# Kernel optimization log

Hardware: AMD Instinct MI355X
Metric: run time of the kernel (lower is better)

The kernel has to match this reference:

```python
import jax, jax.numpy as jnp
import numpy as np

B, K1, N, DIMS = 512, 11, 5, 784  # K1 = K+1 samples per class incl. query
H = 512  # model_size


def _lstm(x_seq, W, U, b):
    """Keras-style LSTM, return_sequences=True.
    x_seq: [B, T, I]; W: [I, 4H]; U: [H, 4H]; b: [4H]. Gate order i,f,g,o.
    """
    units = U.shape[0]
    bsz = x_seq.shape[0]
    # precompute input projections for all timesteps: [T, B, 4H]
    xw = jnp.einsum('bti,ih->tbh', x_seq, W) + b

    def step(carry, xw_t):
        h, c = carry
        z = xw_t + h @ U  # [B, 4H]
        i, f, g, o = jnp.split(z, 4, axis=-1)
        i = jax.nn.sigmoid(i)
        f = jax.nn.sigmoid(f)
        g = jnp.tanh(g)
        o = jax.nn.sigmoid(o)
        c = f * c + i * g
        h = o * jnp.tanh(c)
        return (h, c), h

    init = (jnp.zeros((bsz, units), x_seq.dtype), jnp.zeros((bsz, units), x_seq.dtype))
    _, hs = jax.lax.scan(step, init, xw)  # hs: [T, B, H]
    return jnp.transpose(hs, (1, 0, 2))  # [B, T, H]


def setup_inputs() -> dict:
    key = jax.random.key(0)
    ks = jax.random.split(key, 8)
    return {
        'input_images': jax.random.normal(ks[0], (B, K1, N, DIMS), jnp.float32),
        'input_labels': jax.random.uniform(ks[1], (B, K1, N, N), jnp.float32),
        'W1': jax.random.normal(ks[2], (N + DIMS, 4 * H), jnp.float32) * 0.02,
        'U1': jax.random.normal(ks[3], (H, 4 * H), jnp.float32) * 0.02,
        'b1': jnp.zeros((4 * H,), jnp.float32),
        'W2': jax.random.normal(ks[4], (H, 4 * N), jnp.float32) * 0.02,
        'U2': jax.random.normal(ks[5], (N, 4 * N), jnp.float32) * 0.02,
        'b2': jnp.zeros((4 * N,), jnp.float32),
    }


def reference(input_images, input_labels, W1, U1, b1, W2, U2, b2):
    K = K1 - 1
    support_imgs = input_images[:, :K]               # [B, K, N, D]
    query_imgs = input_images[:, -1].reshape(-1, 1, N, DIMS)  # [B, 1, N, D]
    support_lbls = input_labels[:, :K]               # [B, K, N, N]
    concat_support = jnp.concatenate([support_imgs, support_lbls], axis=-1)
    zero_lbls = jnp.zeros((B, 1, N, N), input_images.dtype)
    concat_query = jnp.concatenate([query_imgs, zero_lbls], axis=-1)
    seq = jnp.concatenate([concat_support, concat_query], axis=1)  # [B, K1, N, N+D]
    seq = seq.reshape(-1, N * K1, N + DIMS)          # [B, T, N+D], T = N*K1
    x = _lstm(seq, W1, U1, b1)                       # [B, T, H]
    out = _lstm(x, W2, U2, b2)                       # [B, T, N]
    return out.reshape(-1, K1, N, N)
```

## Files before the change

kernel.cpp:

```cpp
#include <hip/hip_runtime.h>

typedef __attribute__((ext_vector_type(8))) __bf16 bf16x8;
typedef __attribute__((ext_vector_type(8))) unsigned short ushort8;
typedef __attribute__((ext_vector_type(4))) float f32x4;
typedef __attribute__((ext_vector_type(2))) unsigned long long u64x2;

#define DEVINL __device__ __forceinline__
#define RLX __ATOMIC_RELAXED
#define AGT __HIP_MEMORY_SCOPE_AGENT

constexpr int B_C    = 512;
constexpr int DIMS_C = 784;
constexpr int T_C    = 55;
constexpr int I0_C   = 789;
constexpr int KP_C   = 800;
constexpr int H_C    = 512;
constexpr int G4_C   = 2048;
constexpr int M1_C   = 28160;

constexpr size_t OFF_A    = 0;
constexpr size_t SZ_A     = (size_t)M1_C * KP_C * 2;
constexpr size_t OFF_W1T  = OFF_A + SZ_A;
constexpr size_t SZ_W1T   = (size_t)G4_C * KP_C * 2;
constexpr size_t OFF_U1T  = OFF_W1T + SZ_W1T;
constexpr size_t SZ_U1T   = (size_t)G4_C * H_C * 2;
constexpr size_t OFF_XW1  = OFF_U1T + SZ_U1T;
constexpr size_t SZ_XW1   = (size_t)M1_C * G4_C * 2;
constexpr size_t OFF_H    = OFF_XW1 + SZ_XW1;
constexpr size_t SZ_H     = (size_t)2 * B_C * H_C * 2;
constexpr size_t OFF_XMID = OFF_H + SZ_H;
constexpr size_t SZ_XMID  = (size_t)M1_C * H_C * 4;
constexpr size_t OFF_XW2  = OFF_XMID + SZ_XMID;
constexpr size_t SZ_XW2   = (size_t)M1_C * 20 * 4;
constexpr size_t OFF_W2T  = OFF_XW2 + SZ_XW2;
constexpr size_t SZ_W2T   = (size_t)20 * H_C * 4;
constexpr size_t OFF_CNT  = OFF_W2T + SZ_W2T;

DEVINL unsigned short f2bf(float f) {
  unsigned u = __builtin_bit_cast(unsigned, f);
  u += 0x7fffu + ((u >> 16) & 1u);
  return (unsigned short)(u >> 16);
}
DEVINL float sigm(float x) {
  return __builtin_amdgcn_rcpf(1.f + __builtin_amdgcn_exp2f(-1.4426950408889634f * x));
}
DEVINL float tanh_(float x) {
  return 2.f * __builtin_amdgcn_rcpf(1.f + __builtin_amdgcn_exp2f(-2.8853900817779268f * x)) - 1.f;
}
DEVINL void gl_lds16(const void* g, void* l) {
  __builtin_amdgcn_global_load_lds((const __attribute__((address_space(1))) void*)g,
                                   (__attribute__((address_space(3))) void*)l, 16, 0, 0);
}
DEVINL void gl_lds16_coh(const void* g, void* l) {
  __builtin_amdgcn_global_load_lds((const __attribute__((address_space(1))) void*)g,
                                   (__attribute__((address_space(3))) void*)l, 16, 0, 17);
}


__global__ void pack_a(const float* __restrict__ img, const float* __restrict__ lbl,
                       unsigned short* __restrict__ A) {
  int gid = blockIdx.x * blockDim.x + threadIdx.x;
  constexpr int CPR = KP_C / 8;
  if (gid >= M1_C * CPR) return;
  int r  = gid / CPR;
  int cc = gid - r * CPR;
  int t = r >> 9, b = r & 511;
  int k1 = t / 5, n = t - k1 * 5;
  int c0 = cc * 8;
  ushort8 v;
  if (c0 + 8 <= DIMS_C) {
    const float* p = img + ((size_t)((b * 11 + k1) * 5 + n)) * DIMS_C + c0;
    f32x4 x0 = *(const f32x4*)(p);
    f32x4 x1 = *(const f32x4*)(p + 4);
#pragma unroll
    for (int j = 0; j < 4; ++j) { v[j] = f2bf(x0[j]); v[4 + j] = f2bf(x1[j]); }
  } else {
#pragma unroll
    for (int j = 0; j < 8; ++j) {
      int c = c0 + j;
      float x = 0.f;
      if (c < DIMS_C) x = img[((size_t)((b * 11 + k1) * 5 + n)) * DIMS_C + c];
      else if (c < I0_C && k1 < 10) x = lbl[((size_t)((b * 11 + k1) * 5 + n)) * 5 + (c - DIMS_C)];
      v[j] = f2bf(x);
    }
  }
  *(ushort8*)(A + (size_t)r * KP_C + c0) = v;
}

__global__ void pack_w1t(const float* __restrict__ W1, unsigned short* __restrict__ W1T) {
  int gid = blockIdx.x * blockDim.x + threadIdx.x;
  if (gid >= G4_C * KP_C) return;
  int col = gid / KP_C, k = gid - col * KP_C;
  float x = (k < I0_C) ? W1[(size_t)k * G4_C + col] : 0.f;
  W1T[(size_t)col * KP_C + k] = f2bf(x);
}

__global__ void pack_u1t(const float* __restrict__ U1, unsigned short* __restrict__ U1T) {
  int gid = blockIdx.x * blockDim.x + threadIdx.x;
  if (gid >= G4_C * H_C) return;
  int col = gid / H_C, k = gid - col * H_C;
  U1T[(size_t)col * H_C + k] = f2bf(U1[(size_t)k * G4_C + col]);
}

__global__ void pack_w2t(const float* __restrict__ W2, float* __restrict__ W2T) {
  int gid = blockIdx.x * blockDim.x + threadIdx.x;
  if (gid >= 20 * H_C) return;
  int col = gid / H_C, k = gid - col * H_C;
  W2T[(size_t)col * H_C + k] = W2[(size_t)k * 20 + col];
}

__launch_bounds__(256, 2)
__global__ void gemm1(const unsigned short* __restrict__ A,
                      const unsigned short* __restrict__ Bt,
                      const float* __restrict__ bias,
                      _Float16* __restrict__ C)
{
  __shared__ unsigned short sA[2][128 * 32];
  __shared__ unsigned short sB[2][128 * 32];
  const int tid = threadIdx.x;
  const int w = tid >> 6, l = tid & 63;
  const int lo = l & 15, hi = l >> 4;
  const int wm = w >> 1, wn = w & 1;
  const int id = blockIdx.x;
  const int swz = (id & 7) * 440 + (id >> 3);
  const int by = swz >> 4;
  const int bx = swz & 15;

  const unsigned short* aSrc[2];
  const unsigned short* bSrc[2];
#pragma unroll
  for (int q = 0; q < 2; ++q) {
    int row = w * 32 + q * 16 + (l >> 2);
    int ch = l & 3;
    int sw = (row >> 1) & 3;
    aSrc[q] = A  + (size_t)(by * 128 + row) * KP_C + (ch ^ sw) * 8;
    bSrc[q] = Bt + (size_t)(bx * 128 + row) * KP_C + (ch ^ sw) * 8;
  }
  int aOff[4], bOff[4];
#pragma unroll
  for (int i = 0; i < 4; ++i) {
    int rA = wm * 64 + i * 16 + lo;
    aOff[i] = rA * 32 + ((hi ^ ((rA >> 1) & 3)) * 8);
    int rB = wn * 64 + i * 16 + lo;
    bOff[i] = rB * 32 + ((hi ^ ((rB >> 1) & 3)) * 8);
  }

  f32x4 acc[4][4];
#pragma unroll
  for (int i = 0; i < 4; ++i)
#pragma unroll
    for (int j = 0; j < 4; ++j) acc[i][j] = (f32x4){0.f, 0.f, 0.f, 0.f};

#define G1_STAGE(buf, ks)                                                  \
  {                                                                        \
    _Pragma("unroll")                                                      \
    for (int q = 0; q < 2; ++q) {                                          \
      gl_lds16(aSrc[q] + (ks) * 32, &sA[buf][w * 1024 + q * 512]);         \
      gl_lds16(bSrc[q] + (ks) * 32, &sB[buf][w * 1024 + q * 512]);         \
    }                                                                      \
  }

  G1_STAGE(0, 0);
  asm volatile("s_waitcnt vmcnt(0)" ::: "memory");
  __syncthreads();

  int cur = 0;
#pragma unroll 1
  for (int ks = 0; ks < KP_C / 32; ++ks) {
    if (ks < KP_C / 32 - 1) G1_STAGE(cur ^ 1, ks + 1);
    bf16x8 af[4], bfr[4];
#pragma unroll
    for (int i = 0; i < 4; ++i) {
      af[i]  = *(const bf16x8*)(&sA[cur][0] + aOff[i]);
      bfr[i] = *(const bf16x8*)(&sB[cur][0] + bOff[i]);
    }
#pragma unroll
    for (int mi = 0; mi < 4; ++mi)
#pragma unroll
      for (int ni = 0; ni < 4; ++ni)
        acc[mi][ni] = __builtin_amdgcn_mfma_f32_16x16x32_bf16(af[mi], bfr[ni], acc[mi][ni], 0, 0, 0);
    asm volatile("s_waitcnt vmcnt(0)" ::: "memory");
    __syncthreads();
    cur ^= 1;
  }
#undef G1_STAGE

  const size_t crow0 = (size_t)by * 128 + wm * 64;
  const int ccol0 = bx * 128 + wn * 64;
#pragma unroll
  for (int ni = 0; ni < 4; ++ni) {
    int col = ccol0 + ni * 16 + lo;
    float bv = bias[col];
#pragma unroll
    for (int mi = 0; mi < 4; ++mi) {
#pragma unroll
      for (int j = 0; j < 4; ++j) {
        size_t row = crow0 + mi * 16 + hi * 4 + j;
        C[row * G4_C + col] = (_Float16)(acc[mi][ni][j] + bv);
      }
    }
  }
}

__launch_bounds__(256, 2)
__global__ void lstm1(const _Float16* __restrict__ xw,
                      const unsigned short* __restrict__ U1T,
                      unsigned short* __restrict__ hbuf,
                      float* __restrict__ xmid,
                      unsigned int* __restrict__ cnt)
{
  __shared__ unsigned short sH[16 * 512];
  __shared__ float sG[4 * 16 * 32];

  const int tid = threadIdx.x;
  const int g = tid >> 6;
  const int l = tid & 63;
  const int lo = l & 15, hi = l >> 4;
  const int bg = blockIdx.x >> 4;
  const int cg = blockIdx.x & 15;
  const int brow0 = bg * 16;
  const int ub = cg * 32;

  bf16x8 bu[2][16];
#pragma unroll
  for (int nf = 0; nf < 2; ++nf) {
    const unsigned short* src = U1T + ((size_t)(g * H_C + ub + nf * 16 + lo)) * H_C + hi * 8;
#pragma unroll
    for (int kk = 0; kk < 16; ++kk)
      bu[nf][kk] = *(const bf16x8*)(src + kk * 32);
  }

  const int s0 = lo & 7;
  const int aO0 = lo * 1024;

  const int half = l >> 5;
  const int u = l & 31;
  const int rbase = g * 4 + half * 2;
  const int uread = u ^ (g << 3);

  float c_st[2] = {0.f, 0.f};

  const _Float16* xb = xw + (size_t)(brow0 + rbase) * G4_C + ub + u;
  float xwv[4][2];
#pragma unroll
  for (int g2 = 0; g2 < 4; ++g2)
#pragma unroll
    for (int j = 0; j < 2; ++j)
      xwv[g2][j] = (float)xb[(size_t)j * G4_C + g2 * H_C];

#pragma unroll 1
  for (int t = 0; t < T_C; ++t) {
    f32x4 acc[2];
    acc[0] = (f32x4){0.f, 0.f, 0.f, 0.f};
    acc[1] = (f32x4){0.f, 0.f, 0.f, 0.f};

    if (t > 0) {
      {
        const unsigned* fp = cnt + (size_t)(bg * 16 + (l & 15)) * 16;
        unsigned target = (unsigned)t;
        while (true) {
          unsigned v = __hip_atomic_load(fp, RLX, AGT);
          if (__all(v >= target)) break;
          __builtin_amdgcn_s_sleep(1);
        }
      }
      asm volatile("" ::: "memory");

      const unsigned short* hsrc = hbuf + (size_t)(t & 1) * (B_C * H_C);
#pragma unroll
      for (int p = 0; p < 4; ++p) {
        int row = g * 4 + p;
        gl_lds16_coh(hsrc + (size_t)(brow0 + row) * H_C + ((l ^ (row & 7)) * 8),
                     sH + row * 512);
      }
      asm volatile("s_waitcnt vmcnt(0)" ::: "memory");
      __syncthreads();

#pragma unroll
      for (int kk = 0; kk < 16; ++kk) {
        int off = (((kk * 4 + hi) ^ s0) << 4);
        bf16x8 a0 = *(const bf16x8*)((const char*)sH + aO0 + off);
        acc[0] = __builtin_amdgcn_mfma_f32_16x16x32_bf16(a0, bu[0][kk], acc[0], 0, 0, 0);
        acc[1] = __builtin_amdgcn_mfma_f32_16x16x32_bf16(a0, bu[1][kk], acc[1], 0, 0, 0);
      }
    }

#pragma unroll
    for (int nf = 0; nf < 2; ++nf)
#pragma unroll
      for (int j = 0; j < 4; ++j) {
        int row = hi * 4 + j;
        sG[g * 512 + row * 32 + ((nf * 16 + lo) ^ (hi << 3))] = acc[nf][j];
      }
    __syncthreads();

    float hnew[2];
#pragma unroll
    for (int j = 0; j < 2; ++j) {
      int r = rbase + j;
      float zi = sG[0 * 512 + r * 32 + uread] + xwv[0][j];
      float zf = sG[1 * 512 + r * 32 + uread] + xwv[1][j];
      float zg = sG[2 * 512 + r * 32 + uread] + xwv[2][j];
      float zo = sG[3 * 512 + r * 32 + uread] + xwv[3][j];
      float iv = sigm(zi), fv = sigm(zf), gv = tanh_(zg), ov = sigm(zo);
      float cv = fv * c_st[j] + iv * gv;
      c_st[j] = cv;
      hnew[j] = ov * tanh_(cv);
    }

    if (t < T_C - 1) {
      unsigned short* hd = hbuf + (size_t)((t & 1) ^ 1) * (B_C * H_C);
#pragma unroll
      for (int j = 0; j < 2; ++j) {
        float other = __shfl_xor(hnew[j], 1);
        if ((u & 1) == 0) {
          unsigned val = (unsigned)f2bf(hnew[j]) | ((unsigned)f2bf(other) << 16);
          __hip_atomic_store((unsigned*)(hd + (size_t)(brow0 + rbase + j) * H_C + ub + u), val,
                             RLX, AGT);
        }
      }

      __syncthreads();
      if (tid == 0)
        __hip_atomic_store(&cnt[(size_t)(bg * 16 + cg) * 16], (unsigned)(t + 1), RLX, AGT);

#pragma unroll
      for (int j = 0; j < 2; ++j)
        __builtin_nontemporal_store(hnew[j],
            &xmid[((size_t)t * B_C + brow0 + rbase + j) * H_C + ub + u]);
      const _Float16* xp = xb + (size_t)(t + 1) * B_C * G4_C;
#pragma unroll
      for (int g2 = 0; g2 < 4; ++g2)
#pragma unroll
        for (int j = 0; j < 2; ++j)
          xwv[g2][j] = (float)xp[(size_t)j * G4_C + g2 * H_C];
    } else {
#pragma unroll
      for (int j = 0; j < 2; ++j)
        __builtin_nontemporal_store(hnew[j],
            &xmid[((size_t)t * B_C + brow0 + rbase + j) * H_C + ub + u]);
    }
  }
}

__global__ void gemm2(const float* __restrict__ X,
                      const float* __restrict__ W2T,
                      const float* __restrict__ b2,
                      float* __restrict__ XW2)
{
  int r = blockIdx.x * blockDim.x + threadIdx.x;
  if (r >= M1_C) return;
  float acc[20];
#pragma unroll
  for (int j = 0; j < 20; ++j) acc[j] = b2[j];
  const float* xr = X + (size_t)r * H_C;
  for (int k = 0; k < H_C; k += 4) {
    f32x4 xv = *(const f32x4*)(xr + k);
#pragma unroll
    for (int j = 0; j < 20; ++j) {
      f32x4 wv = *(const f32x4*)(W2T + (size_t)j * H_C + k);
      acc[j] += xv[0]*wv[0] + xv[1]*wv[1] + xv[2]*wv[2] + xv[3]*wv[3];
    }
  }
  float* op = XW2 + (size_t)r * 20;
#pragma unroll
  for (int j = 0; j < 20; ++j) op[j] = acc[j];
}

__global__ void lstm2(const float* __restrict__ XW2,
                      const float* __restrict__ U2,
                      float* __restrict__ out)
{
  int b = blockIdx.x * blockDim.x + threadIdx.x;
  if (b >= B_C) return;
  float u2[5][20];
#pragma unroll
  for (int k = 0; k < 5; ++k)
#pragma unroll
    for (int j = 0; j < 20; ++j) u2[k][j] = U2[k * 20 + j];
  float h[5] = {0, 0, 0, 0, 0}, c[5] = {0, 0, 0, 0, 0};
  for (int t = 0; t < T_C; ++t) {
    const float* xr = XW2 + ((size_t)t * B_C + b) * 20;
    float z[20];
#pragma unroll
    for (int j = 0; j < 20; ++j) z[j] = xr[j];
#pragma unroll
    for (int k = 0; k < 5; ++k) {
      float hk = h[k];
#pragma unroll
      for (int j = 0; j < 20; ++j) z[j] += hk * u2[k][j];
    }
#pragma unroll
    for (int n = 0; n < 5; ++n) {
      float iv = sigm(z[n]), fv = sigm(z[5 + n]), gv = tanh_(z[10 + n]), ov = sigm(z[15 + n]);
      c[n] = fv * c[n] + iv * gv;
      h[n] = ov * tanh_(c[n]);
    }
    int k1 = t / 5, nn = t - k1 * 5;
    float* op = out + (((size_t)b * 11 + k1) * 5 + nn) * 5;
#pragma unroll
    for (int j = 0; j < 5; ++j) op[j] = h[j];
  }
}

extern "C" void kernel_launch(void* const* d_in, const int* in_sizes, int n_in,
                              void* d_out, int out_size, void* d_ws, size_t ws_size,
                              hipStream_t stream) {
  (void)in_sizes; (void)n_in; (void)out_size; (void)ws_size;
  const float* img = (const float*)d_in[0];
  const float* lbl = (const float*)d_in[1];
  const float* W1  = (const float*)d_in[2];
  const float* U1  = (const float*)d_in[3];
  const float* b1  = (const float*)d_in[4];
  const float* W2  = (const float*)d_in[5];
  const float* U2  = (const float*)d_in[6];
  const float* b2  = (const float*)d_in[7];

  char* ws = (char*)d_ws;
  unsigned short* A    = (unsigned short*)(ws + OFF_A);
  unsigned short* W1T  = (unsigned short*)(ws + OFF_W1T);
  unsigned short* U1T  = (unsigned short*)(ws + OFF_U1T);
  _Float16*       XW1  = (_Float16*)      (ws + OFF_XW1);
  unsigned short* HB   = (unsigned short*)(ws + OFF_H);
  float*          XMID = (float*)         (ws + OFF_XMID);
  float*          XW2  = (float*)         (ws + OFF_XW2);
  float*          W2T  = (float*)         (ws + OFF_W2T);
  unsigned int*   CNT  = (unsigned int*)  (ws + OFF_CNT);

  hipMemsetAsync(CNT, 0, 512 * 64, stream);

  pack_a  <<<(M1_C * (KP_C / 8)) / 256, 256, 0, stream>>>(img, lbl, A);
  pack_w1t<<<(G4_C * KP_C) / 256,      256, 0, stream>>>(W1, W1T);
  pack_u1t<<<(G4_C * H_C) / 256,       256, 0, stream>>>(U1, U1T);
  pack_w2t<<<(20 * H_C + 255) / 256,   256, 0, stream>>>(W2, W2T);

  gemm1<<<3520, 256, 0, stream>>>(A, W1T, b1, XW1);
  lstm1<<<512, 256, 0, stream>>>(XW1, U1T, HB, XMID, CNT);
  gemm2<<<(M1_C + 255) / 256, 256, 0, stream>>>(XMID, W2T, b2, XW2);
  lstm2<<<8, 64, 0, stream>>>(XW2, U2, (float*)d_out);
}
```

Baseline: 458.2 us.

## Deepen gemm1 K-tile to 64 with XOR swizzle, split gemm2 columns, prefetch lstm2 inputs

gemm1 now stages 64-wide K slices per iteration instead of 32. The padded K grows to 832, and an 8-way XOR swizzle over 16-byte chunks addresses LDS. This halves the number of barriers and waits per K, but adds padding work and doubles the LDS footprint. gemm2 spreads each row's 20 outputs over 4 threads to get more parallelism, and lstm2 software-prefetches the next timestep's gate inputs into registers so the load latency sits off the serial recurrence.

```diff
diff --git a/kernel.cpp b/kernel.cpp
--- a/kernel.cpp
+++ b/kernel.cpp
@@ -13,7 +13,7 @@
 constexpr int DIMS_C = 784;
 constexpr int T_C    = 55;
 constexpr int I0_C   = 789;
-constexpr int KP_C   = 800;
+constexpr int KP_C   = 832;
 constexpr int H_C    = 512;
 constexpr int G4_C   = 2048;
 constexpr int M1_C   = 28160;
@@ -115,8 +115,8 @@
                       const float* __restrict__ bias,
                       _Float16* __restrict__ C)
 {
-  __shared__ unsigned short sA[2][128 * 32];
-  __shared__ unsigned short sB[2][128 * 32];
+  __shared__ unsigned short sA[2][128 * 64];
+  __shared__ unsigned short sB[2][128 * 64];
   const int tid = threadIdx.x;
   const int w = tid >> 6, l = tid & 63;
   const int lo = l & 15, hi = l >> 4;
@@ -126,23 +126,24 @@
   const int by = swz >> 4;
   const int bx = swz & 15;
 
-  const unsigned short* aSrc[2];
-  const unsigned short* bSrc[2];
-#pragma unroll
-  for (int q = 0; q < 2; ++q) {
-    int row = w * 32 + q * 16 + (l >> 2);
-    int ch = l & 3;
-    int sw = (row >> 1) & 3;
-    aSrc[q] = A  + (size_t)(by * 128 + row) * KP_C + (ch ^ sw) * 8;
-    bSrc[q] = Bt + (size_t)(bx * 128 + row) * KP_C + (ch ^ sw) * 8;
-  }
-  int aOff[4], bOff[4];
+  const unsigned short* aSrc[4];
+  const unsigned short* bSrc[4];
+  int ldsOff[4];
+#pragma unroll
+  for (int q = 0; q < 4; ++q) {
+    int rowb = w * 32 + q * 8;
+    int row = rowb + (l >> 3);
+    int slot = l & 7;
+    int src_chunk = slot ^ (row & 7);
+    aSrc[q] = A  + (size_t)(by * 128 + row) * KP_C + src_chunk * 8;
+    bSrc[q] = Bt + (size_t)(bx * 128 + row) * KP_C + src_chunk * 8;
+    ldsOff[q] = rowb * 64;
+  }
+  int aRow[4], bRow[4];
 #pragma unroll
   for (int i = 0; i < 4; ++i) {
-    int rA = wm * 64 + i * 16 + lo;
-    aOff[i] = rA * 32 + ((hi ^ ((rA >> 1) & 3)) * 8);
-    int rB = wn * 64 + i * 16 + lo;
-    bOff[i] = rB * 32 + ((hi ^ ((rB >> 1) & 3)) * 8);
+    aRow[i] = wm * 64 + i * 16 + lo;
+    bRow[i] = wn * 64 + i * 16 + lo;
   }
 
   f32x4 acc[4][4];
@@ -154,9 +155,9 @@
 #define G1_STAGE(buf, ks)                                                  \
   {                                                                        \
     _Pragma("unroll")                                                      \
-    for (int q = 0; q < 2; ++q) {                                          \
-      gl_lds16(aSrc[q] + (ks) * 32, &sA[buf][w * 1024 + q * 512]);         \
-      gl_lds16(bSrc[q] + (ks) * 32, &sB[buf][w * 1024 + q * 512]);         \
+    for (int q = 0; q < 4; ++q) {                                          \
+      gl_lds16(aSrc[q] + (ks) * 64, &sA[buf][ldsOff[q]]);                  \
+      gl_lds16(bSrc[q] + (ks) * 64, &sB[buf][ldsOff[q]]);                  \
     }                                                                      \
   }
 
@@ -166,19 +167,24 @@
 
   int cur = 0;
 #pragma unroll 1
-  for (int ks = 0; ks < KP_C / 32; ++ks) {
-    if (ks < KP_C / 32 - 1) G1_STAGE(cur ^ 1, ks + 1);
-    bf16x8 af[4], bfr[4];
-#pragma unroll
-    for (int i = 0; i < 4; ++i) {
-      af[i]  = *(const bf16x8*)(&sA[cur][0] + aOff[i]);
-      bfr[i] = *(const bf16x8*)(&sB[cur][0] + bOff[i]);
-    }
-#pragma unroll
-    for (int mi = 0; mi < 4; ++mi)
-#pragma unroll
-      for (int ni = 0; ni < 4; ++ni)
-        acc[mi][ni] = __builtin_amdgcn_mfma_f32_16x16x32_bf16(af[mi], bfr[ni], acc[mi][ni], 0, 0, 0);
+  for (int ks = 0; ks < KP_C / 64; ++ks) {
+    if (ks < KP_C / 64 - 1) G1_STAGE(cur ^ 1, ks + 1);
+#pragma unroll
+    for (int ks2 = 0; ks2 < 2; ++ks2) {
+      bf16x8 af[4], bfr[4];
+#pragma unroll
+      for (int i = 0; i < 4; ++i) {
+        af[i]  = *(const bf16x8*)((const char*)&sA[cur][0] +
+                  aRow[i] * 128 + (((ks2 * 4 + hi) ^ (aRow[i] & 7)) * 16));
+        bfr[i] = *(const bf16x8*)((const char*)&sB[cur][0] +
+                  bRow[i] * 128 + (((ks2 * 4 + hi) ^ (bRow[i] & 7)) * 16));
+      }
+#pragma unroll
+      for (int mi = 0; mi < 4; ++mi)
+#pragma unroll
+        for (int ni = 0; ni < 4; ++ni)
+          acc[mi][ni] = __builtin_amdgcn_mfma_f32_16x16x32_bf16(af[mi], bfr[ni], acc[mi][ni], 0, 0, 0);
+    }
     asm volatile("s_waitcnt vmcnt(0)" ::: "memory");
     __syncthreads();
     cur ^= 1;
@@ -348,23 +354,24 @@
                       const float* __restrict__ b2,
                       float* __restrict__ XW2)
 {
-  int r = blockIdx.x * blockDim.x + threadIdx.x;
-  if (r >= M1_C) return;
-  float acc[20];
-#pragma unroll
-  for (int j = 0; j < 20; ++j) acc[j] = b2[j];
+  int gid = blockIdx.x * blockDim.x + threadIdx.x;
+  if (gid >= M1_C * 4) return;
+  int r = gid >> 2, jq = gid & 3;
   const float* xr = X + (size_t)r * H_C;
+  float acc[5];
+#pragma unroll
+  for (int jj = 0; jj < 5; ++jj) acc[jj] = b2[jq * 5 + jj];
   for (int k = 0; k < H_C; k += 4) {
     f32x4 xv = *(const f32x4*)(xr + k);
 #pragma unroll
-    for (int j = 0; j < 20; ++j) {
-      f32x4 wv = *(const f32x4*)(W2T + (size_t)j * H_C + k);
-      acc[j] += xv[0]*wv[0] + xv[1]*wv[1] + xv[2]*wv[2] + xv[3]*wv[3];
-    }
-  }
-  float* op = XW2 + (size_t)r * 20;
-#pragma unroll
-  for (int j = 0; j < 20; ++j) op[j] = acc[j];
+    for (int jj = 0; jj < 5; ++jj) {
+      f32x4 wv = *(const f32x4*)(W2T + (size_t)(jq * 5 + jj) * H_C + k);
+      acc[jj] += xv[0]*wv[0] + xv[1]*wv[1] + xv[2]*wv[2] + xv[3]*wv[3];
+    }
+  }
+  float* op = XW2 + (size_t)r * 20 + jq * 5;
+#pragma unroll
+  for (int jj = 0; jj < 5; ++jj) op[jj] = acc[jj];
 }
 
 __global__ void lstm2(const float* __restrict__ XW2,
@@ -379,11 +386,24 @@
 #pragma unroll
     for (int j = 0; j < 20; ++j) u2[k][j] = U2[k * 20 + j];
   float h[5] = {0, 0, 0, 0, 0}, c[5] = {0, 0, 0, 0, 0};
+
+  float zbuf[20];
+  {
+    const float* xr = XW2 + (size_t)b * 20;
+#pragma unroll
+    for (int j = 0; j < 20; ++j) zbuf[j] = xr[j];
+  }
+
+#pragma unroll 1
   for (int t = 0; t < T_C; ++t) {
-    const float* xr = XW2 + ((size_t)t * B_C + b) * 20;
     float z[20];
 #pragma unroll
-    for (int j = 0; j < 20; ++j) z[j] = xr[j];
+    for (int j = 0; j < 20; ++j) z[j] = zbuf[j];
+    if (t < T_C - 1) {
+      const float* xn = XW2 + ((size_t)(t + 1) * B_C + b) * 20;
+#pragma unroll
+      for (int j = 0; j < 20; ++j) zbuf[j] = xn[j];
+    }
 #pragma unroll
     for (int k = 0; k < 5; ++k) {
       float hk = h[k];
@@ -436,6 +456,6 @@
 
   gemm1<<<3520, 256, 0, stream>>>(A, W1T, b1, XW1);
   lstm1<<<512, 256, 0, stream>>>(XW1, U1T, HB, XMID, CNT);
-  gemm2<<<(M1_C + 255) / 256, 256, 0, stream>>>(XMID, W2T, b2, XW2);
+  gemm2<<<(M1_C * 4 + 255) / 256, 256, 0, stream>>>(XMID, W2T, b2, XW2);
   lstm2<<<8, 64, 0, stream>>>(XW2, U2, (float*)d_out);
 }
```

New measurement: 513.9 us. +12.2%, slower.

## Split gemm2 columns across four threads, prefetch lstm2 inputs, raise gemm1 occupancy

Applied to the files above, without the earlier changes.

gemm2 now assigns each output row to four threads, each computing five of the twenty columns, so the grid has four times as many threads to hide memory latency on a small-M-by-20 projection. lstm2 software-prefetches the next timestep's gate inputs into registers before doing the current step's math, to overlap the serial recurrence with global loads. gemm1's launch bounds ask for three blocks per SIMD instead of two, which may force register spilling. Together these are three unrelated tweaks across different kernels.

```diff
diff --git a/kernel.cpp b/kernel.cpp
--- a/kernel.cpp
+++ b/kernel.cpp
@@ -109,7 +109,7 @@
   W2T[(size_t)col * H_C + k] = W2[(size_t)k * 20 + col];
 }
 
-__launch_bounds__(256, 2)
+__launch_bounds__(256, 3)
 __global__ void gemm1(const unsigned short* __restrict__ A,
                       const unsigned short* __restrict__ Bt,
                       const float* __restrict__ bias,
@@ -348,23 +348,24 @@
                       const float* __restrict__ b2,
                       float* __restrict__ XW2)
 {
-  int r = blockIdx.x * blockDim.x + threadIdx.x;
-  if (r >= M1_C) return;
-  float acc[20];
-#pragma unroll
-  for (int j = 0; j < 20; ++j) acc[j] = b2[j];
+  int gid = blockIdx.x * blockDim.x + threadIdx.x;
+  if (gid >= M1_C * 4) return;
+  int r = gid >> 2, jq = gid & 3;
   const float* xr = X + (size_t)r * H_C;
+  float acc[5];
+#pragma unroll
+  for (int jj = 0; jj < 5; ++jj) acc[jj] = b2[jq * 5 + jj];
   for (int k = 0; k < H_C; k += 4) {
     f32x4 xv = *(const f32x4*)(xr + k);
 #pragma unroll
-    for (int j = 0; j < 20; ++j) {
-      f32x4 wv = *(const f32x4*)(W2T + (size_t)j * H_C + k);
-      acc[j] += xv[0]*wv[0] + xv[1]*wv[1] + xv[2]*wv[2] + xv[3]*wv[3];
-    }
-  }
-  float* op = XW2 + (size_t)r * 20;
-#pragma unroll
-  for (int j = 0; j < 20; ++j) op[j] = acc[j];
+    for (int jj = 0; jj < 5; ++jj) {
+      f32x4 wv = *(const f32x4*)(W2T + (size_t)(jq * 5 + jj) * H_C + k);
+      acc[jj] += xv[0]*wv[0] + xv[1]*wv[1] + xv[2]*wv[2] + xv[3]*wv[3];
+    }
+  }
+  float* op = XW2 + (size_t)r * 20 + jq * 5;
+#pragma unroll
+  for (int jj = 0; jj < 5; ++jj) op[jj] = acc[jj];
 }
 
 __global__ void lstm2(const float* __restrict__ XW2,
@@ -379,11 +380,24 @@
 #pragma unroll
     for (int j = 0; j < 20; ++j) u2[k][j] = U2[k * 20 + j];
   float h[5] = {0, 0, 0, 0, 0}, c[5] = {0, 0, 0, 0, 0};
+
+  float zbuf[20];
+  {
+    const float* xr = XW2 + (size_t)b * 20;
+#pragma unroll
+    for (int j = 0; j < 20; ++j) zbuf[j] = xr[j];
+  }
+
+#pragma unroll 1
   for (int t = 0; t < T_C; ++t) {
-    const float* xr = XW2 + ((size_t)t * B_C + b) * 20;
     float z[20];
 #pragma unroll
-    for (int j = 0; j < 20; ++j) z[j] = xr[j];
+    for (int j = 0; j < 20; ++j) z[j] = zbuf[j];
+    if (t < T_C - 1) {
+      const float* xn = XW2 + ((size_t)(t + 1) * B_C + b) * 20;
+#pragma unroll
+      for (int j = 0; j < 20; ++j) zbuf[j] = xn[j];
+    }
 #pragma unroll
     for (int k = 0; k < 5; ++k) {
       float hk = h[k];
@@ -436,6 +450,6 @@
 
   gemm1<<<3520, 256, 0, stream>>>(A, W1T, b1, XW1);
   lstm1<<<512, 256, 0, stream>>>(XW1, U1T, HB, XMID, CNT);
-  gemm2<<<(M1_C + 255) / 256, 256, 0, stream>>>(XMID, W2T, b2, XW2);
+  gemm2<<<(M1_C * 4 + 255) / 256, 256, 0, stream>>>(XMID, W2T, b2, XW2);
   lstm2<<<8, 64, 0, stream>>>(XW2, U2, (float*)d_out);
 }
```

Measured after the change: 515.6 us. 1.13x slower.
